# Kernel tuning notes

Measured on AMD Instinct MI355X. Metric: run time of the kernel, lower is better.

Reference implementation:

```python
import jax, jax.numpy as jnp
import numpy as np
import math

B, L, D = 2, 2048, 512
H, HD = 8, 64                      # num_heads, head_dim = D // H
NG = D * (D - 1) // 2              # SO(D) generator count = 130816


def setup_inputs() -> dict:
    key = jax.random.key(0)
    ks = jax.random.split(key, 8)
    x = jax.random.normal(ks[0], (B, L, D), jnp.float32)
    # additive causal mask [L, L]
    mask = jnp.where(jnp.tril(jnp.ones((L, L), bool)), 0.0, -1e9).astype(jnp.float32)
    coef = lambda k: jax.random.normal(k, (NG,), jnp.float32) * 0.1
    basis = lambda k: jax.random.normal(k, (HD, HD), jnp.float32) * 0.1
    return {
        "x": x, "mask": mask,
        "coef_q": coef(ks[1]), "coef_k": coef(ks[2]),
        "coef_v": coef(ks[3]), "coef_o": coef(ks[4]),
        "bias_q": jnp.zeros((D,), jnp.float32), "bias_k": jnp.zeros((D,), jnp.float32),
        "bias_v": jnp.zeros((D,), jnp.float32), "bias_o": jnp.zeros((D,), jnp.float32),
        "basis_q": basis(ks[5]), "basis_k": basis(ks[6]),
    }


def _make_W(coefs):
    # W = I + sum_i coef_i * G_i, with G_i the antisymmetric basis (row-major i<j).
    iu = jnp.triu_indices(D, k=1)
    A = jnp.zeros((D, D), coefs.dtype).at[iu].set(coefs)
    return A - A.T + jnp.eye(D, dtype=coefs.dtype)


def _proj(x, coefs, bias):
    # F.linear(x, W, b) = x @ W.T + b
    return x @ _make_W(coefs).T + bias


def _invariants(t, basis):
    # t: [B, H, L, HD] -> concat(norm, t @ basis.T)[..., :HD]
    norm = jnp.linalg.norm(t, axis=-1, keepdims=True)
    ip = jnp.einsum('bhld,nd->bhln', t, basis)
    return jnp.concatenate([norm, ip], axis=-1)[..., :HD]


def reference(x, mask, coef_q, coef_k, coef_v, coef_o,
              bias_q, bias_k, bias_v, bias_o, basis_q, basis_k):
    split = lambda t: t.reshape(B, L, H, HD).transpose(0, 2, 1, 3)  # [B,H,L,HD]
    Q = split(_proj(x, coef_q, bias_q))
    K = split(_proj(x, coef_k, bias_k))
    V = split(_proj(x, coef_v, bias_v))
    Qi = _invariants(Q, basis_q)
    Ki = _invariants(K, basis_k)
    scores = jnp.einsum('bhld,bhmd->bhlm', Qi, Ki) / math.sqrt(HD) + mask
    attn = jax.nn.softmax(scores, axis=-1)
    out = jnp.einsum('bhlm,bhmd->bhld', attn, V)
    out = out.transpose(0, 2, 1, 3).reshape(B, L, D)
    return _proj(out, coef_o, bias_o)
```

## Files before the change

kernel.cpp:

```cpp
#include <hip/hip_runtime.h>
#include <hip/hip_bf16.h>
#include <math.h>

#define D_ 512
#define B_ 2
#define L_ 2048
#define H_ 8
#define HD_ 64

typedef __attribute__((ext_vector_type(8))) short short8;
typedef __attribute__((ext_vector_type(4))) float f32x4;
typedef _Float16 half8 __attribute__((ext_vector_type(8)));

__device__ __forceinline__ ushort f2bf(float f) {
  __hip_bfloat16 h = __float2bfloat16(f);
  return *(ushort*)&h;
}
__device__ __forceinline__ float bf2f(ushort u) {
  unsigned int v = ((unsigned int)u) << 16;
  union { unsigned int u; float f; } c; c.u = v; return c.f;
}
__device__ __forceinline__ ushort f2h(float f) {
  _Float16 h = (_Float16)f;
  return *(ushort*)&h;
}
__device__ __forceinline__ int swz(int row, int col) {
  return row*64 + (((col>>3) ^ (row&7))<<3) + (col&7);
}
__device__ __forceinline__ int tri_idx(int i, int j) {
  return i*(D_-1) - (i*(i-1))/2 + (j - i - 1);
}

#define GLL16(g, l) __builtin_amdgcn_global_load_lds( \
    (const __attribute__((address_space(1))) void*)(g), \
    (__attribute__((address_space(3))) void*)(l), 16, 0, 0)

__global__ void prep_kernel(const float* __restrict__ x,
                            const float* __restrict__ cq, const float* __restrict__ ck,
                            const float* __restrict__ cv, const float* __restrict__ co,
                            const float* __restrict__ basq, const float* __restrict__ bask,
                            ushort* __restrict__ xb, ushort* __restrict__ Wb,
                            ushort* __restrict__ Bq, ushort* __restrict__ Bk) {
  int blk = blockIdx.x, tid = threadIdx.x;
  if (blk < 2048) {
    int i = (blk*256 + tid)*4;
    float4 v = *(const float4*)(x + i);
    ushort4 o = make_ushort4(f2h(v.x), f2h(v.y), f2h(v.z), f2h(v.w));
    *(ushort4*)(xb + i) = o;
  } else if (blk < 6144) {
    int e = (blk-2048)*256 + tid;
    int m = e >> 18, n = (e>>9)&511, k = e&511;
    const float* cf = (m==0)?cq:(m==1)?ck:(m==2)?cv:co;
    float v = (k>n) ? cf[tri_idx(n,k)] : (k<n) ? -cf[tri_idx(k,n)] : 0.f;
    Wb[e] = f2h(v);
  } else {
    int e = (blk-6144)*256 + tid;
    int which = e >> 12, ee = e & 4095;
    int n = ee >> 6, d = ee & 63;
    const float* bs = which ? bask : basq;
    float v = (n==0) ? 0.f : bs[(n-1)*64 + d];
    (which ? Bk : Bq)[ee] = f2h(v);
  }
}

__global__ __launch_bounds__(256) void proj_qkv_kernel(
    const ushort* __restrict__ Xb, const float* __restrict__ Xf,
    const ushort* __restrict__ Wb,
    const float* __restrict__ bq, const float* __restrict__ bk,
    const float* __restrict__ bv,
    const ushort* __restrict__ Bq, const ushort* __restrict__ Bk,
    ushort* __restrict__ QiO, float* __restrict__ NqV,
    ushort* __restrict__ KiO, float* __restrict__ NkV,
    ushort* __restrict__ Vt_g)
{
  __shared__ ushort BufA[4096];
  __shared__ ushort BufQ[4096];
  __shared__ ushort BufK[4096];
  __shared__ ushort BufV[4096];

  const int tid = threadIdx.x;
  const int lane = tid & 63, w = tid >> 6;
  const int lr = lane & 15, lg = lane >> 4;
  const int h = blockIdx.x, mb = blockIdx.y;
  const int n0 = h*64, m0 = mb*64;
  const ushort* Wq = Wb;
  const ushort* Wk = Wb + 262144;
  const ushort* Wv = Wb + 524288;

  f32x4 accQ[4] = {}, accK[4] = {}, accV[4] = {};
  for (int k0 = 0; k0 < 512; k0 += 64) {
    __syncthreads();
    #pragma unroll
    for (int i = 0; i < 2; ++i) {
      int idx = tid + 256*i;
      int row = idx >> 3, c = idx & 7;
      int so = swz(row, c*8);
      *(short8*)&BufA[so] = *(const short8*)(Xb + (size_t)(m0+row)*512 + k0 + c*8);
      *(short8*)&BufQ[so] = *(const short8*)(Wq + (size_t)(n0+row)*512 + k0 + c*8);
      *(short8*)&BufK[so] = *(const short8*)(Wk + (size_t)(n0+row)*512 + k0 + c*8);
      *(short8*)&BufV[so] = *(const short8*)(Wv + (size_t)(n0+row)*512 + k0 + c*8);
    }
    __syncthreads();
    half8 af[2];
    #pragma unroll
    for (int ks = 0; ks < 2; ++ks)
      af[ks] = *(const half8*)&BufA[swz(w*16+lr, (ks*4+lg)*8)];
    #pragma unroll
    for (int nb = 0; nb < 4; ++nb) {
      #pragma unroll
      for (int ks = 0; ks < 2; ++ks) {
        int so = swz(nb*16+lr, (ks*4+lg)*8);
        accQ[nb] = __builtin_amdgcn_mfma_f32_16x16x32_f16(af[ks], *(const half8*)&BufQ[so], accQ[nb], 0,0,0);
        accK[nb] = __builtin_amdgcn_mfma_f32_16x16x32_f16(af[ks], *(const half8*)&BufK[so], accK[nb], 0,0,0);
        accV[nb] = __builtin_amdgcn_mfma_f32_16x16x32_f16(af[ks], *(const half8*)&BufV[so], accV[nb], 0,0,0);
      }
    }
  }

  float ex[4][4];
  #pragma unroll
  for (int nb = 0; nb < 4; ++nb)
    #pragma unroll
    for (int r = 0; r < 4; ++r) {
      size_t m = m0 + w*16 + lg*4 + r;
      ex[nb][r] = Xf[m*512 + n0 + nb*16 + lr];
    }
  const int b = m0 >> 11;

  #pragma unroll
  for (int nb = 0; nb < 4; ++nb) {
    float bv4 = bv[n0 + nb*16 + lr];
    float v0 = ex[nb][0] + accV[nb][0] + bv4;
    float v1 = ex[nb][1] + accV[nb][1] + bv4;
    float v2 = ex[nb][2] + accV[nb][2] + bv4;
    float v3 = ex[nb][3] + accV[nb][3] + bv4;
    ushort4 o = make_ushort4(f2bf(v0), f2bf(v1), f2bf(v2), f2bf(v3));
    int l0 = (m0 & 2047) + w*16 + lg*4;
    size_t idx = (size_t)(b*8 + h)*131072 + (size_t)(nb*16 + lr)*2048 + l0;
    *(ushort4*)(Vt_g + idx) = o;
  }

  float qQ[4][4], qK[4][4];
  #pragma unroll
  for (int nb = 0; nb < 4; ++nb) {
    float bq4 = bq[n0 + nb*16 + lr];
    float bk4 = bk[n0 + nb*16 + lr];
    #pragma unroll
    for (int r = 0; r < 4; ++r) {
      qQ[nb][r] = ex[nb][r] + accQ[nb][r] + bq4;
      qK[nb][r] = ex[nb][r] + accK[nb][r] + bk4;
    }
  }
  float normQ[4], normK[4];
  #pragma unroll
  for (int r = 0; r < 4; ++r) {
    float sq = 0.f, sk = 0.f;
    #pragma unroll
    for (int nb = 0; nb < 4; ++nb) {
      sq = fmaf(qQ[nb][r], qQ[nb][r], sq);
      sk = fmaf(qK[nb][r], qK[nb][r], sk);
    }
    sq += __shfl_xor(sq, 1, 16); sk += __shfl_xor(sk, 1, 16);
    sq += __shfl_xor(sq, 2, 16); sk += __shfl_xor(sk, 2, 16);
    sq += __shfl_xor(sq, 4, 16); sk += __shfl_xor(sk, 4, 16);
    sq += __shfl_xor(sq, 8, 16); sk += __shfl_xor(sk, 8, 16);
    normQ[r] = sqrtf(sq); normK[r] = sqrtf(sk);
  }
  __syncthreads();
  {
    #pragma unroll
    for (int i = 0; i < 2; ++i) {
      int idx = tid + 256*i;
      int row = idx >> 3, c = idx & 7;
      int so = swz(row, c*8);
      *(short8*)&BufQ[so] = *(const short8*)(Bq + row*64 + c*8);
      *(short8*)&BufK[so] = *(const short8*)(Bk + row*64 + c*8);
    }
  }
  #pragma unroll
  for (int nb = 0; nb < 4; ++nb)
    #pragma unroll
    for (int r = 0; r < 4; ++r) {
      int so = swz(w*16 + lg*4 + r, nb*16 + lr);
      BufA[so] = f2h(qQ[nb][r]);
      BufV[so] = f2h(qK[nb][r]);
    }
  __syncthreads();

  f32x4 acc2Q[4] = {}, acc2K[4] = {};
  half8 aq[2], ak[2];
  #pragma unroll
  for (int ks = 0; ks < 2; ++ks) {
    aq[ks] = *(const half8*)&BufA[swz(w*16+lr, (ks*4+lg)*8)];
    ak[ks] = *(const half8*)&BufV[swz(w*16+lr, (ks*4+lg)*8)];
  }
  #pragma unroll
  for (int nb = 0; nb < 4; ++nb) {
    #pragma unroll
    for (int ks = 0; ks < 2; ++ks) {
      int so = swz(nb*16+lr, (ks*4+lg)*8);
      acc2Q[nb] = __builtin_amdgcn_mfma_f32_16x16x32_f16(aq[ks], *(const half8*)&BufQ[so], acc2Q[nb], 0,0,0);
      acc2K[nb] = __builtin_amdgcn_mfma_f32_16x16x32_f16(ak[ks], *(const half8*)&BufK[so], acc2K[nb], 0,0,0);
    }
  }

  float rnq[4] = {0.f,0.f,0.f,0.f}, rnk[4] = {0.f,0.f,0.f,0.f};
  #pragma unroll
  for (int nb = 0; nb < 4; ++nb)
    #pragma unroll
    for (int r = 0; r < 4; ++r) {
      int ninv = nb*16 + lr;
      int l = (m0 & 2047) + w*16 + lg*4 + r;
      float vq = (ninv == 0) ? normQ[r] : acc2Q[nb][r];
      vq *= 0.125f;
      rnq[r] = fmaf(vq, vq, rnq[r]);
      QiO[((size_t)(b*8 + h)*2048 + l)*64 + ninv] = f2h(vq);
      float vk = (ninv == 0) ? normK[r] : acc2K[nb][r];
      rnk[r] = fmaf(vk, vk, rnk[r]);
      KiO[((size_t)(b*8 + h)*2048 + l)*64 + ninv] = f2h(vk);
    }
  #pragma unroll
  for (int r = 0; r < 4; ++r) {
    float sq = rnq[r], sk = rnk[r];
    sq += __shfl_xor(sq, 1, 16); sk += __shfl_xor(sk, 1, 16);
    sq += __shfl_xor(sq, 2, 16); sk += __shfl_xor(sk, 2, 16);
    sq += __shfl_xor(sq, 4, 16); sk += __shfl_xor(sk, 4, 16);
    sq += __shfl_xor(sq, 8, 16); sk += __shfl_xor(sk, 8, 16);
    if (lr == 0) {
      int l = (m0 & 2047) + w*16 + lg*4 + r;
      NqV[(size_t)(b*8 + h)*2048 + l] = sqrtf(sq);
      NkV[(size_t)(b*8 + h)*2048 + l] = sqrtf(sk);
    }
  }
}

__device__ __forceinline__ void stage_kv(const ushort* __restrict__ Kg,
                                         const ushort* __restrict__ Vg,
                                         ushort* KB, ushort* VB,
                                         int w, int lane) {
  const int r8 = lane >> 3;
  const int cx = (lane & 7) ^ r8;
  #pragma unroll
  for (int s = 0; s < 2; ++s) {
    const int seg = w*2 + s;
    const int row = seg*8 + r8;
    GLL16(Kg + (size_t)row*64 + cx*8,   (char*)KB + seg*1024);
    GLL16(Vg + (size_t)row*2048 + cx*8, (char*)VB + seg*1024);
  }
}

__global__ __launch_bounds__(256) void attn_kernel(
    const ushort* __restrict__ Qi_g, const float* __restrict__ NqV,
    const ushort* __restrict__ Ki_g, const float* __restrict__ NkV,
    const ushort* __restrict__ Vt_g,
    float* __restrict__ PartO, float* __restrict__ PartL)
{
  __shared__ ushort KS[2][4096], VS[2][4096], Pl[4096];

  const int tid = threadIdx.x;
  const int lane = tid & 63, w = tid >> 6;
  const int lr = lane & 15, lg = lane >> 4;
  const int blk = blockIdx.x;
  const int half = blk >> 9;
  const int rem = blk & 511;
  const int g  = rem >> 4;
  const int bh = rem & 15;
  const int qb = (g < 16) ? (31 - g) : (g - 16);
  const int T = qb + 1, mid = (T + 1) >> 1;
  const int lo = half ? mid : 0, hi = half ? T : mid;
  const ushort* Kg0 = Ki_g + (size_t)bh*131072;
  const ushort* Vg0 = Vt_g + (size_t)bh*131072;
  const float*  NkVg = NkV + (size_t)bh*2048;
  const int qg0 = qb*64;
  const int qloc = w*16 + lr;
  const int prow = qloc;

  const size_t qoff = ((size_t)bh*2048 + qg0 + qloc)*64;
  const half8 qf0 = *(const half8*)(Qi_g + qoff + lg*8);
  const half8 qf1 = *(const half8*)(Qi_g + qoff + 32 + lg*8);
  const float nqv = NqV[(size_t)bh*2048 + qg0 + qloc];

  float mk = -1e30f;
  for (int jj = lane; jj < T*64; jj += 64) mk = fmaxf(mk, NkVg[jj]);
  #pragma unroll
  for (int off = 1; off < 64; off <<= 1) mk = fmaxf(mk, __shfl_xor(mk, off));
  const float m_ub = nqv * mk;

  float l_lane = 0.f;
  f32x4 accO[4] = {};

  if (lo < hi)
    stage_kv(Kg0 + (size_t)lo*4096, Vg0 + lo*64, KS[lo&1], VS[lo&1], w, lane);

  for (int jb = lo; jb < hi; ++jb) {
    const int cur = jb & 1;
    if (jb + 1 < hi) {
      stage_kv(Kg0 + (size_t)(jb+1)*4096, Vg0 + (jb+1)*64,
               KS[cur^1], VS[cur^1], w, lane);
      asm volatile("s_waitcnt vmcnt(4)" ::: "memory");
    } else {
      asm volatile("s_waitcnt vmcnt(0)" ::: "memory");
    }
    __builtin_amdgcn_sched_barrier(0);
    __builtin_amdgcn_s_barrier();
    __builtin_amdgcn_sched_barrier(0);

    f32x4 sf[4];
    #pragma unroll
    for (int cb = 0; cb < 4; ++cb) {
      f32x4 a = {0.f,0.f,0.f,0.f};
      half8 k0 = *(const half8*)&KS[cur][swz(cb*16+lr, lg*8)];
      half8 k1 = *(const half8*)&KS[cur][swz(cb*16+lr, (4+lg)*8)];
      a = __builtin_amdgcn_mfma_f32_16x16x32_f16(k0, qf0, a, 0,0,0);
      a = __builtin_amdgcn_mfma_f32_16x16x32_f16(k1, qf1, a, 0,0,0);
      sf[cb] = a;
    }
    if (jb == qb) {
      #pragma unroll
      for (int cb = 0; cb < 4; ++cb)
        #pragma unroll
        for (int r = 0; r < 4; ++r)
          if (cb*16 + lg*4 + r > qloc) sf[cb][r] = -1e30f;
    }

    #pragma unroll
    for (int cb = 0; cb < 4; ++cb)
      #pragma unroll
      for (int r = 0; r < 4; ++r) {
        float p = __expf(sf[cb][r] - m_ub);
        l_lane += p;
        sf[cb][r] = p;
      }
    #pragma unroll
    for (int cb = 0; cb < 4; ++cb) {
      ushort4 pk = make_ushort4(f2bf(sf[cb][0]), f2bf(sf[cb][1]),
                                f2bf(sf[cb][2]), f2bf(sf[cb][3]));
      *(ushort4*)&Pl[swz(prow, cb*16 + lg*4)] = pk;
    }

    short8 pfr[2];
    #pragma unroll
    for (int ks = 0; ks < 2; ++ks)
      pfr[ks] = *(const short8*)&Pl[swz(prow, (ks*4+lg)*8)];
    #pragma unroll
    for (int db = 0; db < 4; ++db) {
      f32x4 a = accO[db];
      short8 v0 = *(const short8*)&VS[cur][swz(db*16+lr, lg*8)];
      short8 v1 = *(const short8*)&VS[cur][swz(db*16+lr, (4+lg)*8)];
      a = __builtin_amdgcn_mfma_f32_16x16x32_bf16(v0, pfr[0], a, 0,0,0);
      a = __builtin_amdgcn_mfma_f32_16x16x32_bf16(v1, pfr[1], a, 0,0,0);
      accO[db] = a;
    }

    __builtin_amdgcn_sched_barrier(0);
    __builtin_amdgcn_s_barrier();
    __builtin_amdgcn_sched_barrier(0);
  }

  l_lane += __shfl_xor(l_lane, 16);
  l_lane += __shfl_xor(l_lane, 32);
  const int pbase = half*512 + bh*32 + qb;
  #pragma unroll
  for (int db = 0; db < 4; ++db)
    *(f32x4*)(PartO + (size_t)pbase*4096 + qloc*64 + db*16 + lg*4) = accO[db];
  if (lg == 0) PartL[pbase*64 + qloc] = l_lane;
}

__global__ __launch_bounds__(256) void proj_o_kernel(
    const float* __restrict__ PartO, const float* __restrict__ PartL,
    const ushort* __restrict__ Wb, const float* __restrict__ bo,
    float* __restrict__ OutF)
{
  __shared__ ushort BufA[4096];
  __shared__ ushort BufB[4096];
  __shared__ float ExactT[64][65];

  const int tid = threadIdx.x;
  const int lane = tid & 63, w = tid >> 6;
  const int lr = lane & 15, lg = lane >> 4;
  const int h = blockIdx.x, mb = blockIdx.y;
  const int n0 = h*64, m0 = mb*64;
  const ushort* Wm = Wb + 3*262144;
  const int b_ = m0 >> 11;
  const int qb_ = (m0 & 2047) >> 6;

  f32x4 acc[4] = {};
  for (int k0 = 0; k0 < 512; k0 += 64) {
    __syncthreads();
    const int hh = k0 >> 6;
    const int bh_ = b_*8 + hh;
    const size_t pb0 = (size_t)(bh_*32 + qb_)*4096;
    const int lbase = (bh_*32 + qb_)*64;
    #pragma unroll
    for (int i = 0; i < 2; ++i) {
      int idx = tid + 256*i;
      int row = idx >> 3, c = idx & 7;
      float l0 = PartL[lbase + row];
      float l1 = PartL[32768 + lbase + row];
      float inv = 1.0f / (l0 + l1);
      const float* s0 = PartO + pb0 + row*64 + c*8;
      const float* s1 = s0 + 2097152;
      float4 a0 = *(const float4*)s0, a1 = *(const float4*)(s0+4);
      float4 c0 = *(const float4*)s1, c1 = *(const float4*)(s1+4);
      float o[8] = {(a0.x+c0.x)*inv, (a0.y+c0.y)*inv, (a0.z+c0.z)*inv, (a0.w+c0.w)*inv,
                    (a1.x+c1.x)*inv, (a1.y+c1.y)*inv, (a1.z+c1.z)*inv, (a1.w+c1.w)*inv};
      if (hh == h) {
        #pragma unroll
        for (int k = 0; k < 8; ++k) ExactT[row][c*8+k] = o[k];
      }
      ushort u[8];
      #pragma unroll
      for (int k = 0; k < 8; ++k) u[k] = f2h(o[k]);
      *(short8*)&BufA[swz(row, c*8)] = *(short8*)u;
      *(short8*)&BufB[swz(row, c*8)] = *(const short8*)(Wm + (size_t)(n0+row)*512 + k0 + c*8);
    }
    __syncthreads();
    half8 af[2];
    #pragma unroll
    for (int ks = 0; ks < 2; ++ks)
      af[ks] = *(const half8*)&BufA[swz(w*16+lr, (ks*4+lg)*8)];
    #pragma unroll
    for (int nb = 0; nb < 4; ++nb) {
      #pragma unroll
      for (int ks = 0; ks < 2; ++ks) {
        half8 bfr = *(const half8*)&BufB[swz(nb*16+lr, (ks*4+lg)*8)];
        acc[nb] = __builtin_amdgcn_mfma_f32_16x16x32_f16(af[ks], bfr, acc[nb], 0,0,0);
      }
    }
  }

  #pragma unroll
  for (int nb = 0; nb < 4; ++nb) {
    float bo4 = bo[n0 + nb*16 + lr];
    #pragma unroll
    for (int r = 0; r < 4; ++r) {
      int row = w*16 + lg*4 + r;
      size_t m = m0 + row;
      OutF[m*512 + n0 + nb*16 + lr] = ExactT[row][nb*16 + lr] + acc[nb][r] + bo4;
    }
  }
}

extern "C" void kernel_launch(void* const* d_in, const int* in_sizes, int n_in,
                              void* d_out, int out_size, void* d_ws, size_t ws_size,
                              hipStream_t stream) {
  const float* x       = (const float*)d_in[0];
  const float* coef_q  = (const float*)d_in[2];
  const float* coef_k  = (const float*)d_in[3];
  const float* coef_v  = (const float*)d_in[4];
  const float* coef_o  = (const float*)d_in[5];
  const float* bias_q  = (const float*)d_in[6];
  const float* bias_k  = (const float*)d_in[7];
  const float* bias_v  = (const float*)d_in[8];
  const float* bias_o  = (const float*)d_in[9];
  const float* basis_q = (const float*)d_in[10];
  const float* basis_k = (const float*)d_in[11];
  float* out = (float*)d_out;

  ushort* xb    = (ushort*)d_ws;
  ushort* Wb    = xb + 2097152;
  ushort* Bq    = Wb + 1048576;
  ushort* Bk    = Bq + 4096;
  ushort* Qi    = Bk + 4096;
  ushort* Ki    = Qi + 2097152;
  ushort* Vt_g  = Ki + 2097152;
  float*  NqV   = (float*)(Vt_g + 2097152);
  float*  NkV   = NqV + 32768;
  float*  PartO = NkV + 32768;
  float*  PartL = PartO + 4194304;

  prep_kernel<<<dim3(6176), 256, 0, stream>>>(x, coef_q, coef_k, coef_v, coef_o,
                                              basis_q, basis_k, xb, Wb, Bq, Bk);

  proj_qkv_kernel<<<dim3(8, 64), 256, 0, stream>>>(xb, x, Wb,
      bias_q, bias_k, bias_v, Bq, Bk, Qi, NqV, Ki, NkV, Vt_g);

  attn_kernel<<<dim3(1024), 256, 0, stream>>>(Qi, NqV, Ki, NkV, Vt_g,
                                              PartO, PartL);

  proj_o_kernel<<<dim3(8, 64), 256, 0, stream>>>(PartO, PartL, Wb, bias_o, out);
}
```

Measured before the change: 82.85 us.

## Double-buffer QKV projection loads, prefetch O-projection inputs, remap attention block order

The QKV projection now stages X and W tiles into double-buffered shared memory with direct global-to-LDS loads. The next k-tile's loads are issued before the current tile's MFMAs, with explicit vmcnt waits and barriers. The output projection prefetches the next head's partial outputs, partial sums and W tile into registers while the current tile is computed. The attention kernel's block index mapping is reordered so consecutive blocks interleave batch-head pairs differently, which could change cache locality. Shared memory for the QKV kernel doubles, which may reduce occupancy.

```diff
diff --git a/kernel.cpp b/kernel.cpp
--- a/kernel.cpp
+++ b/kernel.cpp
@@ -63,6 +63,26 @@
   }
 }
 
+__device__ __forceinline__ void stage_xw(const ushort* __restrict__ Xg,
+                                         const ushort* __restrict__ Wqg,
+                                         const ushort* __restrict__ Wkg,
+                                         const ushort* __restrict__ Wvg,
+                                         ushort* A, ushort* Q, ushort* K, ushort* V,
+                                         int w, int lane) {
+  const int r8 = lane >> 3;
+  const int cx = (lane & 7) ^ r8;
+  #pragma unroll
+  for (int s = 0; s < 2; ++s) {
+    const int seg = w*2 + s;
+    const int row = seg*8 + r8;
+    const size_t go = (size_t)row*512 + cx*8;
+    GLL16(Xg  + go, (char*)A + seg*1024);
+    GLL16(Wqg + go, (char*)Q + seg*1024);
+    GLL16(Wkg + go, (char*)K + seg*1024);
+    GLL16(Wvg + go, (char*)V + seg*1024);
+  }
+}
+
 __global__ __launch_bounds__(256) void proj_qkv_kernel(
     const ushort* __restrict__ Xb, const float* __restrict__ Xf,
     const ushort* __restrict__ Wb,
@@ -73,48 +93,55 @@
     ushort* __restrict__ KiO, float* __restrict__ NkV,
     ushort* __restrict__ Vt_g)
 {
-  __shared__ ushort BufA[4096];
-  __shared__ ushort BufQ[4096];
-  __shared__ ushort BufK[4096];
-  __shared__ ushort BufV[4096];
+  __shared__ ushort BufA[2][4096];
+  __shared__ ushort BufQ[2][4096];
+  __shared__ ushort BufK[2][4096];
+  __shared__ ushort BufV[2][4096];
 
   const int tid = threadIdx.x;
   const int lane = tid & 63, w = tid >> 6;
   const int lr = lane & 15, lg = lane >> 4;
   const int h = blockIdx.x, mb = blockIdx.y;
   const int n0 = h*64, m0 = mb*64;
-  const ushort* Wq = Wb;
-  const ushort* Wk = Wb + 262144;
-  const ushort* Wv = Wb + 524288;
+  const ushort* Xg  = Xb + (size_t)m0*512;
+  const ushort* Wqg = Wb + (size_t)n0*512;
+  const ushort* Wkg = Wb + 262144 + (size_t)n0*512;
+  const ushort* Wvg = Wb + 524288 + (size_t)n0*512;
 
   f32x4 accQ[4] = {}, accK[4] = {}, accV[4] = {};
-  for (int k0 = 0; k0 < 512; k0 += 64) {
-    __syncthreads();
-    #pragma unroll
-    for (int i = 0; i < 2; ++i) {
-      int idx = tid + 256*i;
-      int row = idx >> 3, c = idx & 7;
-      int so = swz(row, c*8);
-      *(short8*)&BufA[so] = *(const short8*)(Xb + (size_t)(m0+row)*512 + k0 + c*8);
-      *(short8*)&BufQ[so] = *(const short8*)(Wq + (size_t)(n0+row)*512 + k0 + c*8);
-      *(short8*)&BufK[so] = *(const short8*)(Wk + (size_t)(n0+row)*512 + k0 + c*8);
-      *(short8*)&BufV[so] = *(const short8*)(Wv + (size_t)(n0+row)*512 + k0 + c*8);
-    }
-    __syncthreads();
+  stage_xw(Xg, Wqg, Wkg, Wvg, BufA[0], BufQ[0], BufK[0], BufV[0], w, lane);
+
+  for (int p = 0; p < 8; ++p) {
+    const int cur = p & 1;
+    if (p < 7) {
+      const int k0 = (p+1)*64;
+      stage_xw(Xg + k0, Wqg + k0, Wkg + k0, Wvg + k0,
+               BufA[cur^1], BufQ[cur^1], BufK[cur^1], BufV[cur^1], w, lane);
+      asm volatile("s_waitcnt vmcnt(8)" ::: "memory");
+    } else {
+      asm volatile("s_waitcnt vmcnt(0)" ::: "memory");
+    }
+    __builtin_amdgcn_sched_barrier(0);
+    __builtin_amdgcn_s_barrier();
+    __builtin_amdgcn_sched_barrier(0);
+
     half8 af[2];
     #pragma unroll
     for (int ks = 0; ks < 2; ++ks)
-      af[ks] = *(const half8*)&BufA[swz(w*16+lr, (ks*4+lg)*8)];
+      af[ks] = *(const half8*)&BufA[cur][swz(w*16+lr, (ks*4+lg)*8)];
     #pragma unroll
     for (int nb = 0; nb < 4; ++nb) {
       #pragma unroll
       for (int ks = 0; ks < 2; ++ks) {
         int so = swz(nb*16+lr, (ks*4+lg)*8);
-        accQ[nb] = __builtin_amdgcn_mfma_f32_16x16x32_f16(af[ks], *(const half8*)&BufQ[so], accQ[nb], 0,0,0);
-        accK[nb] = __builtin_amdgcn_mfma_f32_16x16x32_f16(af[ks], *(const half8*)&BufK[so], accK[nb], 0,0,0);
-        accV[nb] = __builtin_amdgcn_mfma_f32_16x16x32_f16(af[ks], *(const half8*)&BufV[so], accV[nb], 0,0,0);
+        accQ[nb] = __builtin_amdgcn_mfma_f32_16x16x32_f16(af[ks], *(const half8*)&BufQ[cur][so], accQ[nb], 0,0,0);
+        accK[nb] = __builtin_amdgcn_mfma_f32_16x16x32_f16(af[ks], *(const half8*)&BufK[cur][so], accK[nb], 0,0,0);
+        accV[nb] = __builtin_amdgcn_mfma_f32_16x16x32_f16(af[ks], *(const half8*)&BufV[cur][so], accV[nb], 0,0,0);
       }
     }
+    __builtin_amdgcn_sched_barrier(0);
+    __builtin_amdgcn_s_barrier();
+    __builtin_amdgcn_sched_barrier(0);
   }
 
   float ex[4][4];
@@ -173,8 +200,8 @@
       int idx = tid + 256*i;
       int row = idx >> 3, c = idx & 7;
       int so = swz(row, c*8);
-      *(short8*)&BufQ[so] = *(const short8*)(Bq + row*64 + c*8);
-      *(short8*)&BufK[so] = *(const short8*)(Bk + row*64 + c*8);
+      *(short8*)&BufQ[0][so] = *(const short8*)(Bq + row*64 + c*8);
+      *(short8*)&BufK[0][so] = *(const short8*)(Bk + row*64 + c*8);
     }
   }
   #pragma unroll
@@ -182,8 +209,8 @@
     #pragma unroll
     for (int r = 0; r < 4; ++r) {
       int so = swz(w*16 + lg*4 + r, nb*16 + lr);
-      BufA[so] = f2h(qQ[nb][r]);
-      BufV[so] = f2h(qK[nb][r]);
+      BufA[0][so] = f2h(qQ[nb][r]);
+      BufV[0][so] = f2h(qK[nb][r]);
     }
   __syncthreads();
 
@@ -191,16 +218,16 @@
   half8 aq[2], ak[2];
   #pragma unroll
   for (int ks = 0; ks < 2; ++ks) {
-    aq[ks] = *(const half8*)&BufA[swz(w*16+lr, (ks*4+lg)*8)];
-    ak[ks] = *(const half8*)&BufV[swz(w*16+lr, (ks*4+lg)*8)];
+    aq[ks] = *(const half8*)&BufA[0][swz(w*16+lr, (ks*4+lg)*8)];
+    ak[ks] = *(const half8*)&BufV[0][swz(w*16+lr, (ks*4+lg)*8)];
   }
   #pragma unroll
   for (int nb = 0; nb < 4; ++nb) {
     #pragma unroll
     for (int ks = 0; ks < 2; ++ks) {
       int so = swz(nb*16+lr, (ks*4+lg)*8);
-      acc2Q[nb] = __builtin_amdgcn_mfma_f32_16x16x32_f16(aq[ks], *(const half8*)&BufQ[so], acc2Q[nb], 0,0,0);
-      acc2K[nb] = __builtin_amdgcn_mfma_f32_16x16x32_f16(ak[ks], *(const half8*)&BufK[so], acc2K[nb], 0,0,0);
+      acc2Q[nb] = __builtin_amdgcn_mfma_f32_16x16x32_f16(aq[ks], *(const half8*)&BufQ[0][so], acc2Q[nb], 0,0,0);
+      acc2K[nb] = __builtin_amdgcn_mfma_f32_16x16x32_f16(ak[ks], *(const half8*)&BufK[0][so], acc2K[nb], 0,0,0);
     }
   }
 
@@ -261,10 +288,10 @@
   const int lane = tid & 63, w = tid >> 6;
   const int lr = lane & 15, lg = lane >> 4;
   const int blk = blockIdx.x;
-  const int half = blk >> 9;
-  const int rem = blk & 511;
-  const int g  = rem >> 4;
-  const int bh = rem & 15;
+  const int bh = ((blk & 7) << 1) | ((blk >> 3) & 1);
+  const int gh = blk >> 4;
+  const int g  = gh & 31;
+  const int half = gh >> 5;
   const int qb = (g < 16) ? (31 - g) : (g - 16);
   const int T = qb + 1, mid = (T + 1) >> 1;
   const int lo = half ? mid : 0, hi = half ? T : mid;
@@ -384,27 +411,43 @@
   const int b_ = m0 >> 11;
   const int qb_ = (m0 & 2047) >> 6;
 
-  f32x4 acc[4] = {};
-  for (int k0 = 0; k0 < 512; k0 += 64) {
-    __syncthreads();
-    const int hh = k0 >> 6;
-    const int bh_ = b_*8 + hh;
+  float4 r0a[2], r0b[2], r1a[2], r1b[2];
+  float rl0[2], rl1[2];
+  short8 rw[2];
+
+  auto issue = [&](int p) {
+    const int bh_ = b_*8 + p;
     const size_t pb0 = (size_t)(bh_*32 + qb_)*4096;
     const int lbase = (bh_*32 + qb_)*64;
     #pragma unroll
     for (int i = 0; i < 2; ++i) {
       int idx = tid + 256*i;
       int row = idx >> 3, c = idx & 7;
-      float l0 = PartL[lbase + row];
-      float l1 = PartL[32768 + lbase + row];
-      float inv = 1.0f / (l0 + l1);
+      rl0[i] = PartL[lbase + row];
+      rl1[i] = PartL[32768 + lbase + row];
       const float* s0 = PartO + pb0 + row*64 + c*8;
-      const float* s1 = s0 + 2097152;
-      float4 a0 = *(const float4*)s0, a1 = *(const float4*)(s0+4);
-      float4 c0 = *(const float4*)s1, c1 = *(const float4*)(s1+4);
-      float o[8] = {(a0.x+c0.x)*inv, (a0.y+c0.y)*inv, (a0.z+c0.z)*inv, (a0.w+c0.w)*inv,
-                    (a1.x+c1.x)*inv, (a1.y+c1.y)*inv, (a1.z+c1.z)*inv, (a1.w+c1.w)*inv};
-      if (hh == h) {
+      r0a[i] = *(const float4*)s0;
+      r0b[i] = *(const float4*)(s0 + 4);
+      r1a[i] = *(const float4*)(s0 + 2097152);
+      r1b[i] = *(const float4*)(s0 + 2097152 + 4);
+      rw[i] = *(const short8*)(Wm + (size_t)(n0+row)*512 + p*64 + c*8);
+    }
+  };
+
+  issue(0);
+  f32x4 acc[4] = {};
+  for (int p = 0; p < 8; ++p) {
+    __syncthreads();
+    #pragma unroll
+    for (int i = 0; i < 2; ++i) {
+      int idx = tid + 256*i;
+      int row = idx >> 3, c = idx & 7;
+      float inv = 1.0f / (rl0[i] + rl1[i]);
+      float o[8] = {(r0a[i].x+r1a[i].x)*inv, (r0a[i].y+r1a[i].y)*inv,
+                    (r0a[i].z+r1a[i].z)*inv, (r0a[i].w+r1a[i].w)*inv,
+                    (r0b[i].x+r1b[i].x)*inv, (r0b[i].y+r1b[i].y)*inv,
+                    (r0b[i].z+r1b[i].z)*inv, (r0b[i].w+r1b[i].w)*inv};
+      if (p == h) {
         #pragma unroll
         for (int k = 0; k < 8; ++k) ExactT[row][c*8+k] = o[k];
       }
@@ -412,8 +455,9 @@
       #pragma unroll
       for (int k = 0; k < 8; ++k) u[k] = f2h(o[k]);
       *(short8*)&BufA[swz(row, c*8)] = *(short8*)u;
-      *(short8*)&BufB[swz(row, c*8)] = *(const short8*)(Wm + (size_t)(n0+row)*512 + k0 + c*8);
-    }
+      *(short8*)&BufB[swz(row, c*8)] = rw[i];
+    }
+    if (p < 7) issue(p+1);
     __syncthreads();
     half8 af[2];
     #pragma unroll
```

After: 79.93 us. -3.5%, faster.
